# Kernel optimization log

Hardware: AMD Instinct MI355X
Metric: run time of the kernel (lower is better)

The kernel has to match this reference:

```python
import jax, jax.numpy as jnp
import numpy as np

N, E, FIN, EDIM, EMB, H, NL, G = 50000, 800000, 128, 16, 64, 2, 3, 64
HC = H * EMB
INV_SQRT_D = float(1.0 / np.sqrt(EMB))
EPS = 1e-5


def setup_inputs() -> dict:
    key = jax.random.key(0)
    ki = iter(jax.random.split(key, 48))
    def p(shape, s=0.1):
        return jax.random.normal(next(ki), shape, dtype=jnp.float32) * s
    inp = {}
    inp["x"] = jax.random.normal(next(ki), (N, FIN), dtype=jnp.float32)
    inp["edge_attr"] = jax.random.normal(next(ki), (E, EDIM), dtype=jnp.float32)
    inp["edge_index"] = jax.random.randint(next(ki), (2, E), 0, N, dtype=jnp.int32)
    inp["batch_index"] = jnp.sort(jax.random.randint(next(ki), (N,), 0, G, dtype=jnp.int32))
    # conv1 (in = FIN) + transf1 + bn1
    inp["c1_qw"] = p((HC, FIN)); inp["c1_qb"] = p((HC,))
    inp["c1_kw"] = p((HC, FIN)); inp["c1_kb"] = p((HC,))
    inp["c1_vw"] = p((HC, FIN)); inp["c1_vb"] = p((HC,))
    inp["c1_ew"] = p((HC, EDIM))
    inp["c1_skw"] = p((HC, FIN)); inp["c1_skb"] = p((HC,))
    inp["c1_bw"] = p((3 * HC,))
    inp["c1_tw"] = p((EMB, HC)); inp["c1_tb"] = p((EMB,))
    inp["c1_bnw"] = jnp.ones((EMB,), jnp.float32); inp["c1_bnb"] = jnp.zeros((EMB,), jnp.float32)
    # stacked inner layers (in = EMB)
    inp["L_qw"] = p((NL, HC, EMB)); inp["L_qb"] = p((NL, HC))
    inp["L_kw"] = p((NL, HC, EMB)); inp["L_kb"] = p((NL, HC))
    inp["L_vw"] = p((NL, HC, EMB)); inp["L_vb"] = p((NL, HC))
    inp["L_ew"] = p((NL, HC, EDIM))
    inp["L_skw"] = p((NL, HC, EMB)); inp["L_skb"] = p((NL, HC))
    inp["L_bw"] = p((NL, 3 * HC))
    inp["L_tw"] = p((NL, EMB, HC)); inp["L_tb"] = p((NL, EMB))
    inp["L_bnw"] = jnp.ones((NL, EMB), jnp.float32); inp["L_bnb"] = jnp.zeros((NL, EMB), jnp.float32)
    return inp


def transformer_conv(x, ea, src, dst, qw, qb, kw, kb, vw, vb, ew, skw, skb, bw):
    """PyG TransformerConv with edge_dim, concat=True, beta=True, dropout=0."""
    n = x.shape[0]
    q = (x @ qw.T + qb).reshape(n, H, EMB)              # [N,H,C]
    k = ((x @ kw.T + kb)[src]).reshape(-1, H, EMB)       # gather source -> [E,H,C]
    v = ((x @ vw.T + vb)[src]).reshape(-1, H, EMB)
    e = (ea @ ew.T).reshape(-1, H, EMB)                  # edge embedding [E,H,C]
    k = k + e
    alpha = jnp.sum(q[dst] * k, axis=-1) * INV_SQRT_D    # [E,H]
    amax = jax.ops.segment_max(alpha, dst, num_segments=n)
    al = jnp.exp(alpha - amax[dst])
    den = jax.ops.segment_sum(al, dst, num_segments=n)
    al = al / den[dst]                                   # softmax over each target's in-edges
    out = jax.ops.segment_sum((v + e) * al[..., None], dst, num_segments=n).reshape(n, HC)
    x_r = x @ skw.T + skb                                # root/skip transform
    beta = jax.nn.sigmoid(jnp.concatenate([out, x_r, out - x_r], axis=-1) @ bw)  # [N]
    return beta[:, None] * x_r + (1.0 - beta[:, None]) * out


def batch_norm(h, w, b):
    m = h.mean(0)
    v = h.var(0)
    return (h - m) * jax.lax.rsqrt(v + EPS) * w + b


def global_pool(x, batch):
    counts = jax.ops.segment_sum(jnp.ones((x.shape[0],), x.dtype), batch, num_segments=G)
    gmean = jax.ops.segment_sum(x, batch, num_segments=G) / jnp.maximum(counts, 1.0)[:, None]
    gmax = jax.ops.segment_max(x, batch, num_segments=G)
    return jnp.concatenate([gmax, gmean], axis=1)        # [G, 2*EMB]


def reference(x, edge_attr, edge_index, batch_index,
              c1_qw, c1_qb, c1_kw, c1_kb, c1_vw, c1_vb, c1_ew, c1_skw, c1_skb, c1_bw,
              c1_tw, c1_tb, c1_bnw, c1_bnb,
              L_qw, L_qb, L_kw, L_kb, L_vw, L_vb, L_ew, L_skw, L_skb, L_bw,
              L_tw, L_tb, L_bnw, L_bnb):
    src, dst = edge_index[0], edge_index[1]
    h = transformer_conv(x, edge_attr, src, dst, c1_qw, c1_qb, c1_kw, c1_kb,
                         c1_vw, c1_vb, c1_ew, c1_skw, c1_skb, c1_bw)
    h = batch_norm(jax.nn.leaky_relu(h @ c1_tw.T + c1_tb), c1_bnw, c1_bnb)
    gr = jnp.zeros((G, 2 * EMB), h.dtype)
    for i in range(NL):  # small fixed layer count
        h = transformer_conv(h, edge_attr, src, dst, L_qw[i], L_qb[i], L_kw[i], L_kb[i],
                             L_vw[i], L_vb[i], L_ew[i], L_skw[i], L_skb[i], L_bw[i])
        h = batch_norm(jax.nn.leaky_relu(h @ L_tw[i].T + L_tb[i]), L_bnw[i], L_bnb[i])
        gr = gr + global_pool(h, batch_index)
    return gr
```

## Files before the change

### kernel.cpp

```cpp
#include <hip/hip_runtime.h>

#define NN 50000
#define NE 800000
#define FIN 128
#define EDIM 16
#define EMB 64
#define NH 2
#define NLAYERS 3
#define NG 64
#define HCC 128
#define INV_SQRT_D 0.125f
#define EPS_BN 1e-5f
#define SCAN_B 196
#define SCALE_L2E 0.18033688f
#define NRT (NN / 16)

typedef __attribute__((ext_vector_type(8))) short bf16x8;
typedef __attribute__((ext_vector_type(4))) float f32x4;

__device__ __forceinline__ unsigned encf(float f){
  unsigned u = __float_as_uint(f);
  return (u & 0x80000000u) ? ~u : (u | 0x80000000u);
}
__device__ __forceinline__ float decf(unsigned e){
  unsigned u = (e & 0x80000000u) ? (e ^ 0x80000000u) : ~e;
  return __uint_as_float(u);
}
__device__ __forceinline__ unsigned f2bf(float x){
  unsigned u = __float_as_uint(x);
  return (u + 0x7fffu + ((u >> 16) & 1u)) >> 16;
}
__device__ __forceinline__ void f2bf_split(float x, unsigned short* hi, unsigned short* lo){
  unsigned h = f2bf(x);
  float hf = __uint_as_float(h << 16);
  *hi = (unsigned short)h;
  *lo = (unsigned short)f2bf(x - hf);
}
__device__ __forceinline__ size_t fragidx(int tile, int NK, int kk, int lane, int j){
  return (((size_t)tile * NK + kk) * 64 + lane) * 8 + j;
}

__global__ void hist_k(const int* __restrict__ dst, int* __restrict__ deg){
  int i = blockIdx.x * 256 + threadIdx.x;
  if (i < NE) atomicAdd(&deg[dst[i]], 1);
}

__global__ void bounds_k(const int* __restrict__ batch, int* __restrict__ starts){
  int i = blockIdx.x * 256 + threadIdx.x;
  if (i >= NN) return;
  int g = batch[i];
  int gp = (i == 0) ? -1 : batch[i - 1];
  for (int gg = gp + 1; gg <= g; gg++) starts[gg] = i;
  if (i == NN - 1){
    for (int gg = g + 1; gg <= NG; gg++) starts[gg] = NN;
  }
}

__global__ void counts_from_starts_k(const int* __restrict__ starts, int* __restrict__ counts){
  int g = threadIdx.x;
  if (g < NG) counts[g] = starts[g + 1] - starts[g];
}

__global__ void scan1_k(const int* __restrict__ deg, int* __restrict__ bsums){
  __shared__ int lds[256];
  int b = blockIdx.x, t = threadIdx.x;
  int idx = b * 256 + t;
  lds[t] = (idx < NN) ? deg[idx] : 0;
  __syncthreads();
  for (int off = 128; off >= 1; off >>= 1){
    if (t < off) lds[t] += lds[t + off];
    __syncthreads();
  }
  if (t == 0) bsums[b] = lds[0];
}

__global__ void scan2_k(int* __restrict__ bsums){
  __shared__ int lds[256];
  int t = threadIdx.x;
  int v = (t < SCAN_B) ? bsums[t] : 0;
  int x = v;
  lds[t] = x;
  __syncthreads();
  for (int off = 1; off < 256; off <<= 1){
    int y = (t >= off) ? lds[t - off] : 0;
    __syncthreads();
    x += y;
    lds[t] = x;
    __syncthreads();
  }
  if (t < SCAN_B) bsums[t] = x - v;
}

__global__ void scan3_k(const int* __restrict__ degin, const int* __restrict__ bsums,
                        int* __restrict__ row_ptr, int* __restrict__ cur){
  __shared__ int lds[256];
  int b = blockIdx.x, t = threadIdx.x;
  int idx = b * 256 + t;
  int v = (idx < NN) ? degin[idx] : 0;
  int x = v;
  lds[t] = x;
  __syncthreads();
  for (int off = 1; off < 256; off <<= 1){
    int y = (t >= off) ? lds[t - off] : 0;
    __syncthreads();
    x += y;
    lds[t] = x;
    __syncthreads();
  }
  int val = bsums[b] + x - v;
  if (idx <= NN) row_ptr[idx] = val;
  if (idx < NN) cur[idx] = val;
}

__global__ void scatter_k(const int* __restrict__ dst, const int* __restrict__ src,
                          int* __restrict__ cur, int* __restrict__ eid,
                          int* __restrict__ src_s){
  int i = blockIdx.x * 256 + threadIdx.x;
  if (i < NE){
    int p = atomicAdd(&cur[dst[i]], 1);
    eid[p] = i;
    src_s[p] = src[i];
  }
}

__global__ void pack_ea_k(const float* __restrict__ ea, const int* __restrict__ eid,
                          unsigned* __restrict__ eab){
  int i = blockIdx.x * 256 + threadIdx.x;
  if (i >= NE * 2) return;
  int p = i >> 1, half = i & 1;
  int e = eid[p];
  const float* s = ea + (size_t)e * 16 + half * 8;
  float4 a = *(const float4*)(s);
  float4 b = *(const float4*)(s + 4);
  uint4 o;
  o.x = f2bf(a.x) | (f2bf(a.y) << 16);
  o.y = f2bf(a.z) | (f2bf(a.w) << 16);
  o.z = f2bf(b.x) | (f2bf(b.y) << 16);
  o.w = f2bf(b.z) | (f2bf(b.w) << 16);
  ((uint4*)eab)[(size_t)p * 2 + half] = o;
}

__global__ void tobf2_k(const float* __restrict__ in, unsigned short* __restrict__ hi,
                        unsigned short* __restrict__ lo){
  int i = blockIdx.x * 256 + threadIdx.x;
  if (i >= NN * 128) return;
  int n = i >> 7, c = i & 127;
  int rt = n >> 4, rr = n & 15;
  int kk = c >> 5, kg = (c & 31) >> 3, j = c & 7;
  size_t idx = fragidx(rt, 4, kk, kg * 16 + rr, j);
  f2bf_split(in[i], &hi[idx], &lo[idx]);
}

__global__ void pack_all_k(const float* __restrict__ qw, const float* __restrict__ kw,
                           const float* __restrict__ vw, const float* __restrict__ skw,
                           const float* __restrict__ qb, const float* __restrict__ kb,
                           const float* __restrict__ vb, const float* __restrict__ skb,
                           const float* __restrict__ tw, const float* __restrict__ ew,
                           unsigned short* __restrict__ W2h, unsigned short* __restrict__ W2l,
                           float* __restrict__ bp,
                           unsigned short* __restrict__ twh, unsigned short* __restrict__ twl,
                           unsigned short* __restrict__ bdh, unsigned short* __restrict__ bdl,
                           int D){
  int i = blockIdx.x * 256 + threadIdx.x;
  int NK = D / 32;
  if (i < 512 * D){
    int c = i / D, d = i - c * D;
    const float* w = (c < 128) ? qw : (c < 256) ? kw : (c < 384) ? vw : skw;
    int tile = c >> 4, rr = c & 15;
    int kk = d >> 5, kg = (d & 31) >> 3, j = d & 7;
    size_t idx = fragidx(tile, NK, kk, kg * 16 + rr, j);
    f2bf_split(w[(c & 127) * D + d], &W2h[idx], &W2l[idx]);
  }
  if (i < 512){
    const float* b = (i < 128) ? qb : (i < 256) ? kb : (i < 384) ? vb : skb;
    bp[i] = b[i & 127];
  }
  if (i < 64 * 128){
    int col = i >> 7, k = i & 127;
    int ct = col >> 4, rr = col & 15;
    int kk = k >> 5, kg = (k & 31) >> 3, j = k & 7;
    size_t idx = fragidx(ct, 4, kk, kg * 16 + rr, j);
    f2bf_split(tw[i], &twh[idx], &twl[idx]);
  }
  if (i < 32 * 128){
    int k = i >> 7, c = i & 127;
    float val = ((k >> 4) == (c >> 6)) ? ew[c * 16 + (k & 15)] : 0.f;
    int ct = c >> 4, rr = c & 15;
    int kg = k >> 3, j = k & 7;
    size_t idx = ((size_t)(ct * 64 + kg * 16 + rr)) * 8 + j;
    f2bf_split(val, &bdh[idx], &bdl[idx]);
  }
}

__global__ __launch_bounds__(256) void qe_k(const float* __restrict__ qf,
    const float* __restrict__ ew, float* __restrict__ qe){
  __shared__ float ews[2048];
  int t = threadIdx.x;
  for (int i = t; i < 2048; i += 256) ews[i] = ew[i];
  __syncthreads();
  int g = t >> 5;
  int hd = t & 31;
  int h = hd >> 4, d = hd & 15;
  int n = blockIdx.x * 8 + g;
  if (n >= NN) return;
  const float* qp = qf + (size_t)n * 128 + h * 64;
  float s = 0.f;
  #pragma unroll 8
  for (int c = 0; c < 64; c++)
    s += qp[c] * ews[(h * 64 + c) * 16 + d];
  qe[(size_t)n * 32 + hd] = s * SCALE_L2E;
}

template<int D>
__global__ __launch_bounds__(256, 4) void gemm5_k(const unsigned short* __restrict__ A2h,
                                                  const unsigned short* __restrict__ A2l,
                                                  const unsigned short* __restrict__ W2h,
                                                  const unsigned short* __restrict__ W2l,
                                                  const float* __restrict__ bp,
                                                  float* __restrict__ qf,
                                                  unsigned* __restrict__ kvb,
                                                  float* __restrict__ sk){
  const int NK = D / 32;
  int t = threadIdx.x;
  int w = t >> 6, lane = t & 63;
  int brow = blockIdx.x * 64 + w * 16;
  int part = blockIdx.y;
  int r = lane & 15, kg = lane >> 4;
  int rt = brow >> 4; if (rt > NRT - 1) rt = NRT - 1;
  int cb0 = (part == 0) ? 0 : (part == 1) ? 2 : (part == 2) ? 3 : 6;
  int cb1 = (part == 0) ? 1 : (part == 1) ? 4 : (part == 2) ? 5 : 7;
  f32x4 acc0[4], acc1[4];
  #pragma unroll
  for (int tt = 0; tt < 4; tt++){
    acc0[tt] = (f32x4){0.f,0.f,0.f,0.f};
    acc1[tt] = (f32x4){0.f,0.f,0.f,0.f};
  }
  const unsigned short* a2hp = A2h + ((size_t)rt * NK) * 512 + lane * 8;
  const unsigned short* a2lp = A2l + ((size_t)rt * NK) * 512 + lane * 8;
  #pragma unroll
  for (int kk = 0; kk < NK; kk++){
    bf16x8 ah = *(const bf16x8*)(a2hp + kk * 512);
    bf16x8 al = *(const bf16x8*)(a2lp + kk * 512);
    bf16x8 b0h[4], b0l[4], b1h[4], b1l[4];
    #pragma unroll
    for (int tt = 0; tt < 4; tt++){
      size_t i0 = fragidx(cb0 * 4 + tt, NK, kk, lane, 0);
      size_t i1 = fragidx(cb1 * 4 + tt, NK, kk, lane, 0);
      b0h[tt] = *(const bf16x8*)(W2h + i0);
      b0l[tt] = *(const bf16x8*)(W2l + i0);
      b1h[tt] = *(const bf16x8*)(W2h + i1);
      b1l[tt] = *(const bf16x8*)(W2l + i1);
    }
    #pragma unroll
    for (int tt = 0; tt < 4; tt++){
      acc0[tt] = __builtin_amdgcn_mfma_f32_16x16x32_bf16(ah, b0h[tt], acc0[tt], 0, 0, 0);
      acc1[tt] = __builtin_amdgcn_mfma_f32_16x16x32_bf16(ah, b1h[tt], acc1[tt], 0, 0, 0);
      acc0[tt] = __builtin_amdgcn_mfma_f32_16x16x32_bf16(al, b0h[tt], acc0[tt], 0, 0, 0);
      acc1[tt] = __builtin_amdgcn_mfma_f32_16x16x32_bf16(al, b1h[tt], acc1[tt], 0, 0, 0);
      acc0[tt] = __builtin_amdgcn_mfma_f32_16x16x32_bf16(ah, b0l[tt], acc0[tt], 0, 0, 0);
      acc1[tt] = __builtin_amdgcn_mfma_f32_16x16x32_bf16(ah, b1l[tt], acc1[tt], 0, 0, 0);
    }
  }
  int rowbase = brow + kg * 4;
  if (part == 0){
    #pragma unroll
    for (int tt = 0; tt < 4; tt++){
      int ch0 = tt * 16 + r, ch1 = 64 + tt * 16 + r;
      float b0 = bp[ch0], b1 = bp[ch1];
      #pragma unroll
      for (int j = 0; j < 4; j++){
        int row = rowbase + j;
        if (row < NN){
          qf[(size_t)row * 128 + ch0] = acc0[tt][j] + b0;
          qf[(size_t)row * 128 + ch1] = acc1[tt][j] + b1;
        }
      }
    }
  } else if (part == 3){
    #pragma unroll
    for (int tt = 0; tt < 4; tt++){
      int ch0 = tt * 16 + r, ch1 = 64 + tt * 16 + r;
      float b0 = bp[384 + ch0], b1 = bp[384 + ch1];
      #pragma unroll
      for (int j = 0; j < 4; j++){
        int row = rowbase + j;
        if (row < NN){
          sk[(size_t)row * 128 + ch0] = acc0[tt][j] + b0;
          sk[(size_t)row * 128 + ch1] = acc1[tt][j] + b1;
        }
      }
    }
  } else {
    int chbase = (part - 1) * 64;
    #pragma unroll
    for (int tt = 0; tt < 4; tt++){
      int ch = chbase + tt * 16 + r;
      float bk = bp[cb0 * 64 + tt * 16 + r];
      float bv = bp[cb1 * 64 + tt * 16 + r];
      #pragma unroll
      for (int j = 0; j < 4; j++){
        int row = rowbase + j;
        if (row < NN){
          float kk4 = acc0[tt][j] + bk;
          float vv = acc1[tt][j] + bv;
          kvb[(size_t)row * 128 + ch] = f2bf(kk4) | (f2bf(vv) << 16);
        }
      }
    }
  }
}

#define EDGE_STEP(EOFF, MASKED)                                               \
  {                                                                           \
    int e = (EOFF);                                                           \
    int s = __shfl(sv, e);                                                    \
    const unsigned* kp = kvb + (size_t)s * 128 + chb;                         \
    uint4 kv0 = *(const uint4*)(kp);                                          \
    uint4 kv1 = *(const uint4*)(kp + 4);                                      \
    size_t g = (size_t)(beg + cb + e);                                        \
    if (MASKED && g >= NE) g = NE - 1;                                        \
    unsigned eau = eab_u[g * 8 + l8];                                         \
    float ea0 = __uint_as_float(eau << 16);                                   \
    float ea1 = __uint_as_float(eau & 0xffff0000u);                           \
    float k0 = __uint_as_float(kv0.x << 16), v0 = __uint_as_float(kv0.x & 0xffff0000u); \
    float k1 = __uint_as_float(kv0.y << 16), v1 = __uint_as_float(kv0.y & 0xffff0000u); \
    float k2 = __uint_as_float(kv0.z << 16), v2 = __uint_as_float(kv0.z & 0xffff0000u); \
    float k3 = __uint_as_float(kv0.w << 16), v3 = __uint_as_float(kv0.w & 0xffff0000u); \
    float k4 = __uint_as_float(kv1.x << 16), v4 = __uint_as_float(kv1.x & 0xffff0000u); \
    float k5 = __uint_as_float(kv1.y << 16), v5 = __uint_as_float(kv1.y & 0xffff0000u); \
    float k6 = __uint_as_float(kv1.z << 16), v6 = __uint_as_float(kv1.z & 0xffff0000u); \
    float k7 = __uint_as_float(kv1.w << 16), v7 = __uint_as_float(kv1.w & 0xffff0000u); \
    float p = fmaf(q[0], k0, fmaf(q[1], k1, fmaf(q[2], k2, fmaf(q[3], k3,     \
              fmaf(q[4], k4, fmaf(q[5], k5, fmaf(q[6], k6, fmaf(q[7], k7,     \
              fmaf(qe2.x, ea0, qe2.y * ea1)))))))));                          \
    p += __shfl_xor(p, 1); p += __shfl_xor(p, 2); p += __shfl_xor(p, 4);      \
    float w = exp2f(p);                                                       \
    if (MASKED && e >= m) w = 0.f;                                            \
    a0 = fmaf(v0, w, a0); a1 = fmaf(v1, w, a1);                               \
    a2 = fmaf(v2, w, a2); a3 = fmaf(v3, w, a3);                               \
    a4 = fmaf(v4, w, a4); a5 = fmaf(v5, w, a5);                               \
    a6 = fmaf(v6, w, a6); a7 = fmaf(v7, w, a7);                               \
    den += w; t0 = fmaf(ea0, w, t0); t1 = fmaf(ea1, w, t1);                   \
  }

__global__ __launch_bounds__(256) void edge_k(const float* __restrict__ qf,
    const unsigned* __restrict__ kvb, const unsigned* __restrict__ eab_u,
    const float* __restrict__ qe, const int* __restrict__ row_ptr,
    const int* __restrict__ src_s, float* __restrict__ accp,
    float* __restrict__ tbuf, float* __restrict__ dbuf){
  int n = (blockIdx.x * 256 + threadIdx.x) >> 6;
  if (n >= NN) return;
  int lane = threadIdx.x & 63;
  int grp = lane >> 4;
  int l8 = lane & 7;
  int chb = ((lane >> 3) & 1) * 64 + l8 * 8;
  int h = (lane >> 3) & 1;
  float q[8];
  {
    float4 qa = *(const float4*)(qf + (size_t)n * 128 + chb);
    float4 qb = *(const float4*)(qf + (size_t)n * 128 + chb + 4);
    q[0] = qa.x * SCALE_L2E; q[1] = qa.y * SCALE_L2E;
    q[2] = qa.z * SCALE_L2E; q[3] = qa.w * SCALE_L2E;
    q[4] = qb.x * SCALE_L2E; q[5] = qb.y * SCALE_L2E;
    q[6] = qb.z * SCALE_L2E; q[7] = qb.w * SCALE_L2E;
  }
  float2 qe2 = *(const float2*)(qe + (size_t)n * 32 + h * 16 + 2 * l8);
  int beg = row_ptr[n], end = row_ptr[n + 1];
  int nb = end - beg;
  float a0=0.f,a1=0.f,a2=0.f,a3=0.f,a4=0.f,a5=0.f,a6=0.f,a7=0.f;
  float den = 0.f, t0 = 0.f, t1 = 0.f;
  for (int cb = 0; cb < nb; cb += 64){
    int sv = (cb + lane < nb) ? src_s[beg + cb + lane] : 0;
    int m = min(64, nb - cb);
    int u = 0;
    for (; u + 8 <= m; u += 8){
      EDGE_STEP(u + grp, false)
      EDGE_STEP(u + 4 + grp, false)
    }
    int rem = m - u;
    if (rem > 0){
      EDGE_STEP(u + grp, true)
      if (rem > 4){
        EDGE_STEP(u + 4 + grp, true)
      }
    }
  }
  a0 += __shfl_xor(a0, 16); a0 += __shfl_xor(a0, 32);
  a1 += __shfl_xor(a1, 16); a1 += __shfl_xor(a1, 32);
  a2 += __shfl_xor(a2, 16); a2 += __shfl_xor(a2, 32);
  a3 += __shfl_xor(a3, 16); a3 += __shfl_xor(a3, 32);
  a4 += __shfl_xor(a4, 16); a4 += __shfl_xor(a4, 32);
  a5 += __shfl_xor(a5, 16); a5 += __shfl_xor(a5, 32);
  a6 += __shfl_xor(a6, 16); a6 += __shfl_xor(a6, 32);
  a7 += __shfl_xor(a7, 16); a7 += __shfl_xor(a7, 32);
  den += __shfl_xor(den, 16); den += __shfl_xor(den, 32);
  t0 += __shfl_xor(t0, 16); t0 += __shfl_xor(t0, 32);
  t1 += __shfl_xor(t1, 16); t1 += __shfl_xor(t1, 32);
  if (lane < 16){
    float4 o0 = {a0, a1, a2, a3};
    float4 o1 = {a4, a5, a6, a7};
    *(float4*)(accp + (size_t)n * 128 + chb) = o0;
    *(float4*)(accp + (size_t)n * 128 + chb + 4) = o1;
    *(float2*)(tbuf + (size_t)n * 32 + h * 16 + 2 * l8) = make_float2(t0, t1);
    if (l8 == 0) dbuf[(size_t)n * 2 + h] = den;
  }
}

__global__ __launch_bounds__(256) void combine2_k(const float* __restrict__ accp,
    const float* __restrict__ sk, const float* __restrict__ bw,
    const unsigned short* __restrict__ twh, const unsigned short* __restrict__ twl,
    const float* __restrict__ tb, const unsigned short* __restrict__ bdh,
    const unsigned short* __restrict__ bdl, const float* __restrict__ tbuf,
    const float* __restrict__ dbuf, float* __restrict__ h2, float* __restrict__ bn_acc){
  __shared__ float ext[64][132];
  __shared__ bf16x8 afh[4][4][64];
  __shared__ bf16x8 afl[4][4][64];
  __shared__ float bws[384];
  __shared__ float bsum[64], bsq[64];
  int t = threadIdx.x;
  int w = t >> 6, lane = t & 63;
  for (int i = t; i < 384; i += 256) bws[i] = bw[i];
  if (t < 64){ bsum[t] = 0.f; bsq[t] = 0.f; }
  {
    int row = lane & 15, kg = lane >> 4;
    int nrow = blockIdx.x * 64 + w * 16 + row;
    if (nrow >= NN) nrow = NN - 1;
    float4 tva = *(const float4*)(tbuf + (size_t)nrow * 32 + kg * 8);
    float4 tvb = *(const float4*)(tbuf + (size_t)nrow * 32 + kg * 8 + 4);
    float tv[8] = {tva.x, tva.y, tva.z, tva.w, tvb.x, tvb.y, tvb.z, tvb.w};
    bf16x8 th, tlw;
    #pragma unroll
    for (int j = 0; j < 8; j++){
      unsigned hb = f2bf(tv[j]);
      th[j] = (short)hb;
      tlw[j] = (short)f2bf(tv[j] - __uint_as_float(hb << 16));
    }
    #pragma unroll
    for (int ct = 0; ct < 8; ct++){
      f32x4 ae = (f32x4){0.f,0.f,0.f,0.f};
      size_t idx = ((size_t)(ct * 64 + lane)) * 8;
      bf16x8 bh = *(const bf16x8*)(bdh + idx);
      bf16x8 bl = *(const bf16x8*)(bdl + idx);
      ae = __builtin_amdgcn_mfma_f32_16x16x32_bf16(th, bh, ae, 0, 0, 0);
      ae = __builtin_amdgcn_mfma_f32_16x16x32_bf16(tlw, bh, ae, 0, 0, 0);
      ae = __builtin_amdgcn_mfma_f32_16x16x32_bf16(th, bl, ae, 0, 0, 0);
      #pragma unroll
      for (int j = 0; j < 4; j++)
        ext[w * 16 + kg * 4 + j][ct * 16 + row] = ae[j];
    }
  }
  int nl = t >> 2, q = t & 3;
  int n = blockIdx.x * 64 + nl;
  bool valid = n < NN;
  float o[32], r[32];
  if (valid){
    const float* ap = accp + (size_t)n * 128 + q * 32;
    const float* sp = sk   + (size_t)n * 128 + q * 32;
    #pragma unroll
    for (int i = 0; i < 32; i += 4){
      float4 va = *(const float4*)(ap + i);
      float4 vr = *(const float4*)(sp + i);
      o[i] = va.x; o[i+1] = va.y; o[i+2] = va.z; o[i+3] = va.w;
      r[i] = vr.x; r[i+1] = vr.y; r[i+2] = vr.z; r[i+3] = vr.w;
    }
  } else {
    #pragma unroll
    for (int i = 0; i < 32; i++){ o[i] = 0.f; r[i] = 0.f; }
  }
  float dh = valid ? dbuf[(size_t)n * 2 + (q >> 1)] : 0.f;
  float invden = dh > 0.f ? 1.f / dh : 0.f;
  __syncthreads();
  #pragma unroll
  for (int i = 0; i < 32; i++)
    o[i] = (o[i] + ext[nl][q * 32 + i]) * invden;
  float pp = 0.f;
  #pragma unroll
  for (int i = 0; i < 32; i++){
    int c = q * 32 + i;
    pp += o[i] * bws[c] + r[i] * bws[128 + c] + (o[i] - r[i]) * bws[256 + c];
  }
  pp += __shfl_xor(pp, 1); pp += __shfl_xor(pp, 2);
  float beta = 1.f / (1.f + __expf(-pp));
  int w2 = t >> 6;
  int r0 = (t & 63) >> 2;
  #pragma unroll
  for (int kg = 0; kg < 4; kg++){
    bf16x8 hv, lv;
    #pragma unroll
    for (int j = 0; j < 8; j++){
      int i = kg * 8 + j;
      float hc = o[i] + beta * (r[i] - o[i]);
      unsigned hb = f2bf(hc);
      hv[j] = (short)hb;
      lv[j] = (short)f2bf(hc - __uint_as_float(hb << 16));
    }
    afh[w2][q][kg * 16 + r0] = hv;
    afl[w2][q][kg * 16 + r0] = lv;
  }
  __syncthreads();
  bf16x8 ah[4], al[4];
  #pragma unroll
  for (int kk = 0; kk < 4; kk++){ ah[kk] = afh[w][kk][lane]; al[kk] = afl[w][kk][lane]; }
  int brow = blockIdx.x * 64 + w * 16;
  #pragma unroll
  for (int ct = 0; ct < 4; ct++){
    f32x4 acc = (f32x4){0.f,0.f,0.f,0.f};
    #pragma unroll
    for (int kk = 0; kk < 4; kk++){
      size_t idx = (((size_t)(ct * 4 + kk)) * 64 + lane) * 8;
      bf16x8 bh = *(const bf16x8*)(twh + idx);
      bf16x8 bl = *(const bf16x8*)(twl + idx);
      acc = __builtin_amdgcn_mfma_f32_16x16x32_bf16(ah[kk], bh, acc, 0, 0, 0);
      acc = __builtin_amdgcn_mfma_f32_16x16x32_bf16(al[kk], bh, acc, 0, 0, 0);
      acc = __builtin_amdgcn_mfma_f32_16x16x32_bf16(ah[kk], bl, acc, 0, 0, 0);
    }
    int col = ct * 16 + (lane & 15);
    float bias = tb[col];
    float ps = 0.f, pq = 0.f;
    #pragma unroll
    for (int j = 0; j < 4; j++){
      int row = brow + (lane >> 4) * 4 + j;
      float s = acc[j] + bias;
      float v = s > 0.f ? s : 0.01f * s;
      if (row < NN){
        h2[(size_t)row * 64 + col] = v;
        ps += v; pq += v * v;
      }
    }
    ps += __shfl_xor(ps, 16); ps += __shfl_xor(ps, 32);
    pq += __shfl_xor(pq, 16); pq += __shfl_xor(pq, 32);
    if (lane < 16){
      atomicAdd(&bsum[col], ps);
      atomicAdd(&bsq[col], pq);
    }
  }
  __syncthreads();
  if (t < 64){
    atomicAdd(&bn_acc[t], bsum[t]);
    atomicAdd(&bn_acc[64 + t], bsq[t]);
  }
}

__global__ void bn_final_k(const float* __restrict__ bn_acc, const float* __restrict__ bnw,
                           const float* __restrict__ bnb, float* __restrict__ ss){
  int j = threadIdx.x;
  if (j < 64){
    float m = bn_acc[j] / (float)NN;
    float v = bn_acc[64 + j] / (float)NN - m * m;
    float sc = bnw[j] * rsqrtf(v + EPS_BN);
    ss[j] = sc;
    ss[64 + j] = bnb[j] - m * sc;
  }
}

__global__ __launch_bounds__(256) void bn_apply_k(const float* __restrict__ h2,
    const float* __restrict__ ss, const int* __restrict__ batch,
    unsigned short* __restrict__ hbh, unsigned short* __restrict__ hbl,
    float* __restrict__ gsum, unsigned* __restrict__ gmax,
    int do_pool){
  int wid = (blockIdx.x * 256 + threadIdx.x) >> 6;
  int lane = threadIdx.x & 63;
  const int CH = (NN + 1023) / 1024;
  int start = wid * CH;
  int end = start + CH; if (end > NN) end = NN;
  float sc = ss[lane], sh = ss[64 + lane];
  int kk = lane >> 5, kg = (lane & 31) >> 3, j = lane & 7;
  int curg = -1; float lmax = 0.f, lsum = 0.f;
  for (int n = start; n < end; n++){
    float v = h2[(size_t)n * 64 + lane] * sc + sh;
    size_t idx = fragidx((n >> 4), 2, kk, kg * 16 + (n & 15), j);
    f2bf_split(v, &hbh[idx], &hbl[idx]);
    if (do_pool){
      int g = batch[n];
      if (g != curg){
        if (curg >= 0){
          atomicAdd(&gsum[curg * 64 + lane], lsum);
          atomicMax(&gmax[curg * 64 + lane], encf(lmax));
        }
        curg = g; lmax = v; lsum = v;
      } else {
        lmax = fmaxf(lmax, v); lsum += v;
      }
    }
  }
  if (do_pool && curg >= 0){
    atomicAdd(&gsum[curg * 64 + lane], lsum);
    atomicMax(&gmax[curg * 64 + lane], encf(lmax));
  }
}

__global__ void pool_final_k(const float* __restrict__ gsum, const unsigned* __restrict__ gmax,
                             const int* __restrict__ counts, float* __restrict__ gr){
  int i = blockIdx.x * 256 + threadIdx.x;
  if (i < NG * 64){
    int g = i >> 6, j = i & 63;
    unsigned e = gmax[i];
    float mx = e ? decf(e) : 0.f;
    int c = counts[g]; if (c < 1) c = 1;
    gr[g * 128 + j]       += mx;
    gr[g * 128 + 64 + j]  += gsum[i] / (float)c;
  }
}

extern "C" void kernel_launch(void* const* d_in, const int* in_sizes, int n_in,
                              void* d_out, int out_size, void* d_ws, size_t ws_size,
                              hipStream_t stream){
  const float* x     = (const float*)d_in[0];
  const float* ea    = (const float*)d_in[1];
  const int*   eidx  = (const int*)d_in[2];
  const int*   batch = (const int*)d_in[3];
  const float* c1_qw = (const float*)d_in[4];
  const float* c1_qb = (const float*)d_in[5];
  const float* c1_kw = (const float*)d_in[6];
  const float* c1_kb = (const float*)d_in[7];
  const float* c1_vw = (const float*)d_in[8];
  const float* c1_vb = (const float*)d_in[9];
  const float* c1_ew = (const float*)d_in[10];
  const float* c1_skw= (const float*)d_in[11];
  const float* c1_skb= (const float*)d_in[12];
  const float* c1_bw = (const float*)d_in[13];
  const float* c1_tw = (const float*)d_in[14];
  const float* c1_tb = (const float*)d_in[15];
  const float* c1_bnw= (const float*)d_in[16];
  const float* c1_bnb= (const float*)d_in[17];
  const float* L_qw  = (const float*)d_in[18];
  const float* L_qb  = (const float*)d_in[19];
  const float* L_kw  = (const float*)d_in[20];
  const float* L_kb  = (const float*)d_in[21];
  const float* L_vw  = (const float*)d_in[22];
  const float* L_vb  = (const float*)d_in[23];
  const float* L_ew  = (const float*)d_in[24];
  const float* L_skw = (const float*)d_in[25];
  const float* L_skb = (const float*)d_in[26];
  const float* L_bw  = (const float*)d_in[27];
  const float* L_tw  = (const float*)d_in[28];
  const float* L_tb  = (const float*)d_in[29];
  const float* L_bnw = (const float*)d_in[30];
  const float* L_bnb = (const float*)d_in[31];
  const int* srcs = eidx;
  const int* dsts = eidx + NE;

  char* p = (char*)d_ws;
  auto carve = [&](size_t bytes) -> void* {
    void* r = (void*)p;
    p += (bytes + 255) & ~(size_t)255;
    return r;
  };
  unsigned short* Wh = (unsigned short*)carve(512 * 128 * sizeof(unsigned short));
  unsigned short* Wl = (unsigned short*)carve(512 * 128 * sizeof(unsigned short));
  float*    bp     = (float*)carve(512 * sizeof(float));
  unsigned short* twph = (unsigned short*)carve(64 * 128 * sizeof(unsigned short));
  unsigned short* twpl = (unsigned short*)carve(64 * 128 * sizeof(unsigned short));
  unsigned short* bdh = (unsigned short*)carve(32 * 128 * sizeof(unsigned short));
  unsigned short* bdl = (unsigned short*)carve(32 * 128 * sizeof(unsigned short));
  float*    qf     = (float*)carve((size_t)NN * 128 * sizeof(float));
  float*    skb_   = (float*)carve((size_t)NN * 128 * sizeof(float));
  unsigned* kvb    = (unsigned*)carve((size_t)NN * 128 * sizeof(unsigned));
  unsigned* eab    = (unsigned*)carve((size_t)NE * 8 * sizeof(unsigned));
  float*    qe     = (float*)carve((size_t)NN * 32 * sizeof(float));
  float*    attn   = (float*)carve((size_t)NN * 128 * sizeof(float));
  float*    tbuf   = (float*)carve((size_t)NN * 32 * sizeof(float));
  float*    dbuf   = (float*)carve((size_t)NN * 2 * sizeof(float));
  unsigned short* xbh = (unsigned short*)carve((size_t)NN * FIN * sizeof(unsigned short));
  unsigned short* xbl = (unsigned short*)carve((size_t)NN * FIN * sizeof(unsigned short));
  unsigned short* hbh = (unsigned short*)carve((size_t)NN * 64 * sizeof(unsigned short));
  unsigned short* hbl = (unsigned short*)carve((size_t)NN * 64 * sizeof(unsigned short));
  float*    h2     = (float*)carve((size_t)NN * 64 * sizeof(float));
  float*    bn_acc4 = (float*)carve(4 * 128 * sizeof(float));
  float*    gsum3  = (float*)carve(3 * (size_t)NG * 64 * sizeof(float));
  unsigned* gmax3  = (unsigned*)carve(3 * (size_t)NG * 64 * sizeof(unsigned));
  float*    ss     = (float*)carve(128 * sizeof(float));
  int*      deg    = (int*)carve(NN * sizeof(int));
  int*      row_ptr= (int*)carve((NN + 1) * sizeof(int));
  int*      eid    = (int*)carve((size_t)NE * sizeof(int));
  int*      src_s  = (int*)carve((size_t)NE * sizeof(int));
  int*      counts = (int*)carve(NG * sizeof(int));
  int*      starts = (int*)carve((NG + 1) * sizeof(int));
  int*      bsums  = (int*)carve(256 * sizeof(int));

  size_t zero_bytes = (4 * 128 * sizeof(float) + 255 & ~(size_t)255)
                    + (3 * (size_t)NG * 64 * sizeof(float) + 255 & ~(size_t)255)
                    + (3 * (size_t)NG * 64 * sizeof(unsigned) + 255 & ~(size_t)255);
  hipMemsetAsync(d_out, 0, (size_t)out_size * sizeof(float), stream);
  hipMemsetAsync(deg, 0, NN * sizeof(int), stream);
  hipMemsetAsync(bn_acc4, 0, zero_bytes, stream);
  hist_k<<<(NE + 255) / 256, 256, 0, stream>>>(dsts, deg);
  bounds_k<<<(NN + 255) / 256, 256, 0, stream>>>(batch, starts);
  counts_from_starts_k<<<1, 64, 0, stream>>>(starts, counts);
  scan1_k<<<SCAN_B, 256, 0, stream>>>(deg, bsums);
  scan2_k<<<1, 256, 0, stream>>>(bsums);
  scan3_k<<<SCAN_B, 256, 0, stream>>>(deg, bsums, row_ptr, deg);
  scatter_k<<<(NE + 255) / 256, 256, 0, stream>>>(dsts, srcs, deg, eid, src_s);
  pack_ea_k<<<(NE * 2 + 255) / 256, 256, 0, stream>>>(ea, eid, eab);
  tobf2_k<<<(NN * FIN + 255) / 256, 256, 0, stream>>>(x, xbh, xbl);

  const unsigned short* hin_h = xbh;
  const unsigned short* hin_l = xbl;
  for (int L = 0; L < 4; L++){
    int D = (L == 0) ? FIN : EMB;
    const float *qw,*qb,*kw,*kb,*vw,*vb,*eww,*skw,*skb,*bww,*tw,*tb,*bnw,*bnb;
    if (L == 0){
      qw=c1_qw; qb=c1_qb; kw=c1_kw; kb=c1_kb; vw=c1_vw; vb=c1_vb;
      eww=c1_ew; skw=c1_skw; skb=c1_skb; bww=c1_bw; tw=c1_tw; tb=c1_tb;
      bnw=c1_bnw; bnb=c1_bnb;
    } else {
      int i = L - 1;
      qw = L_qw + (size_t)i * HCC * EMB;  qb = L_qb + (size_t)i * HCC;
      kw = L_kw + (size_t)i * HCC * EMB;  kb = L_kb + (size_t)i * HCC;
      vw = L_vw + (size_t)i * HCC * EMB;  vb = L_vb + (size_t)i * HCC;
      eww= L_ew + (size_t)i * HCC * EDIM;
      skw= L_skw+ (size_t)i * HCC * EMB;  skb= L_skb+ (size_t)i * HCC;
      bww= L_bw + (size_t)i * 3 * HCC;
      tw = L_tw + (size_t)i * EMB * HCC;  tb = L_tb + (size_t)i * EMB;
      bnw= L_bnw+ (size_t)i * EMB;        bnb= L_bnb+ (size_t)i * EMB;
    }
    float* bn_acc = bn_acc4 + L * 128;
    float* gsum = gsum3 + (size_t)(L > 0 ? L - 1 : 0) * NG * 64;
    unsigned* gmax = gmax3 + (size_t)(L > 0 ? L - 1 : 0) * NG * 64;
    pack_all_k<<<256, 256, 0, stream>>>(qw, kw, vw, skw, qb, kb, vb, skb, tw, eww,
                                        Wh, Wl, bp, twph, twpl, bdh, bdl, D);
    dim3 gg((NN + 63) / 64, 4);
    if (D == 128) gemm5_k<128><<<gg, 256, 0, stream>>>(hin_h, hin_l, Wh, Wl, bp, qf, kvb, skb_);
    else          gemm5_k<64><<<gg, 256, 0, stream>>>(hin_h, hin_l, Wh, Wl, bp, qf, kvb, skb_);
    qe_k<<<(NN + 7) / 8, 256, 0, stream>>>(qf, eww, qe);
    edge_k<<<(NN * 64 + 255) / 256, 256, 0, stream>>>(qf, kvb, eab, qe, row_ptr, src_s, attn, tbuf, dbuf);
    combine2_k<<<(NN + 63) / 64, 256, 0, stream>>>(attn, skb_, bww, twph, twpl, tb, bdh, bdl, tbuf, dbuf, h2, bn_acc);
    bn_final_k<<<1, 64, 0, stream>>>(bn_acc, bnw, bnb, ss);
    bn_apply_k<<<256, 256, 0, stream>>>(h2, ss, batch, hbh, hbl, gsum, gmax, (L > 0) ? 1 : 0);
    if (L > 0) pool_final_k<<<(NG * 64 + 255) / 256, 256, 0, stream>>>(gsum, gmax, counts, (float*)d_out);
    hin_h = hbh; hin_l = hbl;
  }
}
```

Before: 901.7 us.

## Fold batchnorm into next-layer weights and fuse qe into QKV gemm

Batchnorm scale/shift of the previous layer is folded into the packed Q/K/V/skip weights and biases, so combine writes bf16 hi/lo fragments directly and the separate bn_apply pass disappears. The qe projection is computed inside the gemm epilogue from a shared-memory tile instead of a separate kernel re-reading q. Q is stored as scaled bf16 rather than fp32, and pooling finalization is done once for all layers. This cuts several full-node-array passes and launches, at the cost of extra shared memory in the gemm and reduced precision for q.

```diff
diff --git a/kernel.cpp b/kernel.cpp
--- a/kernel.cpp
+++ b/kernel.cpp
@@ -156,6 +156,7 @@
                            const float* __restrict__ qb, const float* __restrict__ kb,
                            const float* __restrict__ vb, const float* __restrict__ skb,
                            const float* __restrict__ tw, const float* __restrict__ ew,
+                           const float* __restrict__ ss, int use_ss,
                            unsigned short* __restrict__ W2h, unsigned short* __restrict__ W2l,
                            float* __restrict__ bp,
                            unsigned short* __restrict__ twh, unsigned short* __restrict__ twl,
@@ -166,14 +167,25 @@
   if (i < 512 * D){
     int c = i / D, d = i - c * D;
     const float* w = (c < 128) ? qw : (c < 256) ? kw : (c < 384) ? vw : skw;
+    float wv = w[(c & 127) * D + d];
+    if (use_ss) wv *= ss[d];
     int tile = c >> 4, rr = c & 15;
     int kk = d >> 5, kg = (d & 31) >> 3, j = d & 7;
     size_t idx = fragidx(tile, NK, kk, kg * 16 + rr, j);
-    f2bf_split(w[(c & 127) * D + d], &W2h[idx], &W2l[idx]);
+    f2bf_split(wv, &W2h[idx], &W2l[idx]);
   }
   if (i < 512){
     const float* b = (i < 128) ? qb : (i < 256) ? kb : (i < 384) ? vb : skb;
-    bp[i] = b[i & 127];
+    const float* w = (i < 128) ? qw : (i < 256) ? kw : (i < 384) ? vw : skw;
+    float bb = b[i & 127];
+    if (use_ss){
+      float acc = 0.f;
+      const float* wr = w + (size_t)(i & 127) * 64;
+      #pragma unroll 8
+      for (int c = 0; c < 64; c++) acc += wr[c] * ss[64 + c];
+      bb += acc;
+    }
+    bp[i] = bb;
   }
   if (i < 64 * 128){
     int col = i >> 7, k = i & 127;
@@ -192,34 +204,19 @@
   }
 }
 
-__global__ __launch_bounds__(256) void qe_k(const float* __restrict__ qf,
-    const float* __restrict__ ew, float* __restrict__ qe){
-  __shared__ float ews[2048];
-  int t = threadIdx.x;
-  for (int i = t; i < 2048; i += 256) ews[i] = ew[i];
-  __syncthreads();
-  int g = t >> 5;
-  int hd = t & 31;
-  int h = hd >> 4, d = hd & 15;
-  int n = blockIdx.x * 8 + g;
-  if (n >= NN) return;
-  const float* qp = qf + (size_t)n * 128 + h * 64;
-  float s = 0.f;
-  #pragma unroll 8
-  for (int c = 0; c < 64; c++)
-    s += qp[c] * ews[(h * 64 + c) * 16 + d];
-  qe[(size_t)n * 32 + hd] = s * SCALE_L2E;
-}
-
 template<int D>
-__global__ __launch_bounds__(256, 4) void gemm5_k(const unsigned short* __restrict__ A2h,
+__global__ __launch_bounds__(256, 4) void gemm6_k(const unsigned short* __restrict__ A2h,
                                                   const unsigned short* __restrict__ A2l,
                                                   const unsigned short* __restrict__ W2h,
                                                   const unsigned short* __restrict__ W2l,
                                                   const float* __restrict__ bp,
-                                                  float* __restrict__ qf,
+                                                  const float* __restrict__ ew,
+                                                  unsigned short* __restrict__ qb16,
+                                                  float* __restrict__ qe,
                                                   unsigned* __restrict__ kvb,
                                                   float* __restrict__ sk){
+  __shared__ float qs[64][128];
+  __shared__ float ews[2048];
   const int NK = D / 32;
   int t = threadIdx.x;
   int w = t >> 6, lane = t & 63;
@@ -263,6 +260,7 @@
   }
   int rowbase = brow + kg * 4;
   if (part == 0){
+    for (int i = t; i < 2048; i += 256) ews[i] = ew[i];
     #pragma unroll
     for (int tt = 0; tt < 4; tt++){
       int ch0 = tt * 16 + r, ch1 = 64 + tt * 16 + r;
@@ -270,11 +268,28 @@
       #pragma unroll
       for (int j = 0; j < 4; j++){
         int row = rowbase + j;
+        float v0 = acc0[tt][j] + b0;
+        float v1 = acc1[tt][j] + b1;
+        qs[w * 16 + kg * 4 + j][ch0] = v0;
+        qs[w * 16 + kg * 4 + j][ch1] = v1;
         if (row < NN){
-          qf[(size_t)row * 128 + ch0] = acc0[tt][j] + b0;
-          qf[(size_t)row * 128 + ch1] = acc1[tt][j] + b1;
+          qb16[(size_t)row * 128 + ch0] = (unsigned short)f2bf(v0 * SCALE_L2E);
+          qb16[(size_t)row * 128 + ch1] = (unsigned short)f2bf(v1 * SCALE_L2E);
         }
       }
+    }
+    __syncthreads();
+    #pragma unroll
+    for (int i = 0; i < 8; i++){
+      int idx = t + 256 * i;
+      int nl = idx >> 5, hd = idx & 31;
+      int h = hd >> 4, d = hd & 15;
+      float s = 0.f;
+      #pragma unroll 8
+      for (int c = 0; c < 64; c++)
+        s += qs[nl][h * 64 + c] * ews[(h * 64 + c) * 16 + d];
+      int n = blockIdx.x * 64 + nl;
+      if (n < NN) qe[(size_t)n * 32 + hd] = s * SCALE_L2E;
     }
   } else if (part == 3){
     #pragma unroll
@@ -343,7 +358,7 @@
     den += w; t0 = fmaf(ea0, w, t0); t1 = fmaf(ea1, w, t1);                   \
   }
 
-__global__ __launch_bounds__(256) void edge_k(const float* __restrict__ qf,
+__global__ __launch_bounds__(256) void edge_k(const unsigned short* __restrict__ qb16,
     const unsigned* __restrict__ kvb, const unsigned* __restrict__ eab_u,
     const float* __restrict__ qe, const int* __restrict__ row_ptr,
     const int* __restrict__ src_s, float* __restrict__ accp,
@@ -353,16 +368,15 @@
   int lane = threadIdx.x & 63;
   int grp = lane >> 4;
   int l8 = lane & 7;
-  int chb = ((lane >> 3) & 1) * 64 + l8 * 8;
   int h = (lane >> 3) & 1;
+  int chb = h * 64 + l8 * 8;
   float q[8];
   {
-    float4 qa = *(const float4*)(qf + (size_t)n * 128 + chb);
-    float4 qb = *(const float4*)(qf + (size_t)n * 128 + chb + 4);
-    q[0] = qa.x * SCALE_L2E; q[1] = qa.y * SCALE_L2E;
-    q[2] = qa.z * SCALE_L2E; q[3] = qa.w * SCALE_L2E;
-    q[4] = qb.x * SCALE_L2E; q[5] = qb.y * SCALE_L2E;
-    q[6] = qb.z * SCALE_L2E; q[7] = qb.w * SCALE_L2E;
+    uint4 qv = *(const uint4*)(qb16 + (size_t)n * 128 + chb);
+    q[0] = __uint_as_float(qv.x << 16); q[1] = __uint_as_float(qv.x & 0xffff0000u);
+    q[2] = __uint_as_float(qv.y << 16); q[3] = __uint_as_float(qv.y & 0xffff0000u);
+    q[4] = __uint_as_float(qv.z << 16); q[5] = __uint_as_float(qv.z & 0xffff0000u);
+    q[6] = __uint_as_float(qv.w << 16); q[7] = __uint_as_float(qv.w & 0xffff0000u);
   }
   float2 qe2 = *(const float2*)(qe + (size_t)n * 32 + h * 16 + 2 * l8);
   int beg = row_ptr[n], end = row_ptr[n + 1];
@@ -406,12 +420,14 @@
   }
 }
 
-__global__ __launch_bounds__(256) void combine2_k(const float* __restrict__ accp,
+__global__ __launch_bounds__(256) void combine3_k(const float* __restrict__ accp,
     const float* __restrict__ sk, const float* __restrict__ bw,
     const unsigned short* __restrict__ twh, const unsigned short* __restrict__ twl,
     const float* __restrict__ tb, const unsigned short* __restrict__ bdh,
     const unsigned short* __restrict__ bdl, const float* __restrict__ tbuf,
-    const float* __restrict__ dbuf, float* __restrict__ h2, float* __restrict__ bn_acc){
+    const float* __restrict__ dbuf, unsigned short* __restrict__ hbh,
+    unsigned short* __restrict__ hbl, float* __restrict__ h2,
+    float* __restrict__ bn_acc, int do_pool){
   __shared__ float ext[64][132];
   __shared__ bf16x8 afh[4][4][64];
   __shared__ bf16x8 afl[4][4][64];
@@ -502,6 +518,7 @@
   #pragma unroll
   for (int kk = 0; kk < 4; kk++){ ah[kk] = afh[w][kk][lane]; al[kk] = afl[w][kk][lane]; }
   int brow = blockIdx.x * 64 + w * 16;
+  int tile = blockIdx.x * 4 + w;
   #pragma unroll
   for (int ct = 0; ct < 4; ct++){
     f32x4 acc = (f32x4){0.f,0.f,0.f,0.f};
@@ -516,14 +533,22 @@
     }
     int col = ct * 16 + (lane & 15);
     float bias = tb[col];
+    int kk2 = col >> 5, kg2 = (col & 31) >> 3, jj = col & 7;
     float ps = 0.f, pq = 0.f;
     #pragma unroll
     for (int j = 0; j < 4; j++){
-      int row = brow + (lane >> 4) * 4 + j;
+      int rr = (lane >> 4) * 4 + j;
+      int row = brow + rr;
       float s = acc[j] + bias;
       float v = s > 0.f ? s : 0.01f * s;
+      if (tile < NRT){
+        size_t fidx = fragidx(tile, 2, kk2, kg2 * 16 + rr, jj);
+        unsigned hb = f2bf(v);
+        hbh[fidx] = (unsigned short)hb;
+        hbl[fidx] = (unsigned short)f2bf(v - __uint_as_float(hb << 16));
+      }
       if (row < NN){
-        h2[(size_t)row * 64 + col] = v;
+        if (do_pool) h2[(size_t)row * 64 + col] = v;
         ps += v; pq += v * v;
       }
     }
@@ -553,53 +578,50 @@
   }
 }
 
-__global__ __launch_bounds__(256) void bn_apply_k(const float* __restrict__ h2,
+__global__ __launch_bounds__(256) void pool_scan_k(const float* __restrict__ h2,
     const float* __restrict__ ss, const int* __restrict__ batch,
-    unsigned short* __restrict__ hbh, unsigned short* __restrict__ hbl,
-    float* __restrict__ gsum, unsigned* __restrict__ gmax,
-    int do_pool){
+    float* __restrict__ gsum, unsigned* __restrict__ gmax){
   int wid = (blockIdx.x * 256 + threadIdx.x) >> 6;
   int lane = threadIdx.x & 63;
   const int CH = (NN + 1023) / 1024;
   int start = wid * CH;
   int end = start + CH; if (end > NN) end = NN;
   float sc = ss[lane], sh = ss[64 + lane];
-  int kk = lane >> 5, kg = (lane & 31) >> 3, j = lane & 7;
   int curg = -1; float lmax = 0.f, lsum = 0.f;
   for (int n = start; n < end; n++){
     float v = h2[(size_t)n * 64 + lane] * sc + sh;
-    size_t idx = fragidx((n >> 4), 2, kk, kg * 16 + (n & 15), j);
-    f2bf_split(v, &hbh[idx], &hbl[idx]);
-    if (do_pool){
-      int g = batch[n];
-      if (g != curg){
-        if (curg >= 0){
-          atomicAdd(&gsum[curg * 64 + lane], lsum);
-          atomicMax(&gmax[curg * 64 + lane], encf(lmax));
-        }
-        curg = g; lmax = v; lsum = v;
-      } else {
-        lmax = fmaxf(lmax, v); lsum += v;
+    int g = batch[n];
+    if (g != curg){
+      if (curg >= 0){
+        atomicAdd(&gsum[curg * 64 + lane], lsum);
+        atomicMax(&gmax[curg * 64 + lane], encf(lmax));
       }
-    }
-  }
-  if (do_pool && curg >= 0){
+      curg = g; lmax = v; lsum = v;
+    } else {
+      lmax = fmaxf(lmax, v); lsum += v;
+    }
+  }
+  if (curg >= 0){
     atomicAdd(&gsum[curg * 64 + lane], lsum);
     atomicMax(&gmax[curg * 64 + lane], encf(lmax));
   }
 }
 
-__global__ void pool_final_k(const float* __restrict__ gsum, const unsigned* __restrict__ gmax,
-                             const int* __restrict__ counts, float* __restrict__ gr){
+__global__ void pool_final_all_k(const float* __restrict__ gsum3, const unsigned* __restrict__ gmax3,
+                                 const int* __restrict__ counts, float* __restrict__ gr){
   int i = blockIdx.x * 256 + threadIdx.x;
-  if (i < NG * 64){
-    int g = i >> 6, j = i & 63;
-    unsigned e = gmax[i];
-    float mx = e ? decf(e) : 0.f;
-    int c = counts[g]; if (c < 1) c = 1;
-    gr[g * 128 + j]       += mx;
-    gr[g * 128 + 64 + j]  += gsum[i] / (float)c;
-  }
+  if (i >= NG * 64) return;
+  int g = i >> 6, j = i & 63;
+  int c = counts[g]; if (c < 1) c = 1;
+  float msum = 0.f, ssum = 0.f;
+  #pragma unroll
+  for (int L = 0; L < 3; L++){
+    unsigned e = gmax3[(size_t)L * NG * 64 + i];
+    msum += e ? decf(e) : 0.f;
+    ssum += gsum3[(size_t)L * NG * 64 + i] / (float)c;
+  }
+  gr[g * 128 + j]      += msum;
+  gr[g * 128 + 64 + j] += ssum;
 }
 
 extern "C" void kernel_launch(void* const* d_in, const int* in_sizes, int n_in,
@@ -653,7 +675,7 @@
   unsigned short* twpl = (unsigned short*)carve(64 * 128 * sizeof(unsigned short));
   unsigned short* bdh = (unsigned short*)carve(32 * 128 * sizeof(unsigned short));
   unsigned short* bdl = (unsigned short*)carve(32 * 128 * sizeof(unsigned short));
-  float*    qf     = (float*)carve((size_t)NN * 128 * sizeof(float));
+  unsigned short* qb16 = (unsigned short*)carve((size_t)NN * 128 * sizeof(unsigned short));
   float*    skb_   = (float*)carve((size_t)NN * 128 * sizeof(float));
   unsigned* kvb    = (unsigned*)carve((size_t)NN * 128 * sizeof(unsigned));
   unsigned* eab    = (unsigned*)carve((size_t)NE * 8 * sizeof(unsigned));
@@ -678,9 +700,9 @@
   int*      starts = (int*)carve((NG + 1) * sizeof(int));
   int*      bsums  = (int*)carve(256 * sizeof(int));
 
-  size_t zero_bytes = (4 * 128 * sizeof(float) + 255 & ~(size_t)255)
-                    + (3 * (size_t)NG * 64 * sizeof(float) + 255 & ~(size_t)255)
-                    + (3 * (size_t)NG * 64 * sizeof(unsigned) + 255 & ~(size_t)255);
+  size_t zero_bytes = ((4 * 128 * sizeof(float) + 255) & ~(size_t)255)
+                    + ((3 * (size_t)NG * 64 * sizeof(float) + 255) & ~(size_t)255)
+                    + ((3 * (size_t)NG * 64 * sizeof(unsigned) + 255) & ~(size_t)255);
   hipMemsetAsync(d_out, 0, (size_t)out_size * sizeof(float), stream);
   hipMemsetAsync(deg, 0, NN * sizeof(int), stream);
   hipMemsetAsync(bn_acc4, 0, zero_bytes, stream);
@@ -715,19 +737,21 @@
       bnw= L_bnw+ (size_t)i * EMB;        bnb= L_bnb+ (size_t)i * EMB;
     }
     float* bn_acc = bn_acc4 + L * 128;
-    float* gsum = gsum3 + (size_t)(L > 0 ? L - 1 : 0) * NG * 64;
-    unsigned* gmax = gmax3 + (size_t)(L > 0 ? L - 1 : 0) * NG * 64;
+    int pl = (L > 0) ? L - 1 : 0;
+    float* gsum = gsum3 + (size_t)pl * NG * 64;
+    unsigned* gmax = gmax3 + (size_t)pl * NG * 64;
     pack_all_k<<<256, 256, 0, stream>>>(qw, kw, vw, skw, qb, kb, vb, skb, tw, eww,
+                                        ss, (L > 0) ? 1 : 0,
                                         Wh, Wl, bp, twph, twpl, bdh, bdl, D);
     dim3 gg((NN + 63) / 64, 4);
-    if (D == 128) gemm5_k<128><<<gg, 256, 0, stream>>>(hin_h, hin_l, Wh, Wl, bp, qf, kvb, skb_);
-    else          gemm5_k<64><<<gg, 256, 0, stream>>>(hin_h, hin_l, Wh, Wl, bp, qf, kvb, skb_);
-    qe_k<<<(NN + 7) / 8, 256, 0, stream>>>(qf, eww, qe);
-    edge_k<<<(NN * 64 + 255) / 256, 256, 0, stream>>>(qf, kvb, eab, qe, row_ptr, src_s, attn, tbuf, dbuf);
-    combine2_k<<<(NN + 63) / 64, 256, 0, stream>>>(attn, skb_, bww, twph, twpl, tb, bdh, bdl, tbuf, dbuf, h2, bn_acc);
+    if (D == 128) gemm6_k<128><<<gg, 256, 0, stream>>>(hin_h, hin_l, Wh, Wl, bp, eww, qb16, qe, kvb, skb_);
+    else          gemm6_k<64><<<gg, 256, 0, stream>>>(hin_h, hin_l, Wh, Wl, bp, eww, qb16, qe, kvb, skb_);
+    edge_k<<<(NN * 64 + 255) / 256, 256, 0, stream>>>(qb16, kvb, eab, qe, row_ptr, src_s, attn, tbuf, dbuf);
+    combine3_k<<<(NN + 63) / 64, 256, 0, stream>>>(attn, skb_, bww, twph, twpl, tb, bdh, bdl,
+                                                   tbuf, dbuf, hbh, hbl, h2, bn_acc, (L > 0) ? 1 : 0);
     bn_final_k<<<1, 64, 0, stream>>>(bn_acc, bnw, bnb, ss);
-    bn_apply_k<<<256, 256, 0, stream>>>(h2, ss, batch, hbh, hbl, gsum, gmax, (L > 0) ? 1 : 0);
-    if (L > 0) pool_final_k<<<(NG * 64 + 255) / 256, 256, 0, stream>>>(gsum, gmax, counts, (float*)d_out);
+    if (L > 0) pool_scan_k<<<256, 256, 0, stream>>>(h2, ss, batch, gsum, gmax);
     hin_h = hbh; hin_l = hbl;
   }
-}
+  pool_final_all_k<<<(NG * 64 + 255) / 256, 256, 0, stream>>>(gsum3, gmax3, counts, (float*)d_out);
+}
```

Measured after the change: 806.9 us. 1.12x faster.
